# Kernel tuning notes

Measured on AMD Instinct MI355X. Metric: run time of the kernel, lower is better.

## Reference

```python
import jax, jax.numpy as jnp
import numpy as np

B, S, TK, N = 16, 32, 128, 512  # batch, sentences, tokens/sentence, 2*hidden_dim


def setup_inputs() -> dict:
    key = jax.random.key(0)
    ks = jax.random.split(key, 10)
    h = jax.random.normal(ks[0], (B, S, TK, N), dtype=jnp.float32)
    s_t_hat = jax.random.normal(ks[1], (B, N), dtype=jnp.float32)
    coverage = jax.random.uniform(ks[2], (B, S, TK), dtype=jnp.float32)
    # binary padding mask (mostly ones)
    enc_padding_mask = (jax.random.uniform(ks[3], (B, S, TK)) > 0.1).astype(jnp.float32)
    beta = jax.random.uniform(ks[4], (B, S), dtype=jnp.float32)
    sc = 1.0 / np.sqrt(N).astype(np.float32)
    W_h = jax.random.normal(ks[5], (N, N), dtype=jnp.float32) * sc   # Linear(N,N,bias=False)
    W_c = jax.random.normal(ks[6], (N,), dtype=jnp.float32)          # Linear(1,N,bias=False) weight[:,0]
    W_d = jax.random.normal(ks[7], (N, N), dtype=jnp.float32) * sc   # decode_proj weight
    b_d = jax.random.normal(ks[8], (N,), dtype=jnp.float32) * sc     # decode_proj bias
    v = jax.random.normal(ks[9], (N,), dtype=jnp.float32) * sc       # v weight[0]
    return {"s_t_hat": s_t_hat, "h": h, "coverage": coverage,
            "enc_padding_mask": enc_padding_mask, "beta": beta,
            "W_h": W_h, "W_c": W_c, "W_d": W_d, "b_d": b_d, "v": v}


def reference(s_t_hat, h, coverage, enc_padding_mask, beta, W_h, W_c, W_d, b_d, v):
    b, s, t_k, n = h.shape
    # encoder features: (b,s,t_k,n) @ W_h^T
    encoder_feature = jnp.einsum('bstn,mn->bstm', h, W_h)
    # decoder projection, broadcast over (s, t_k)
    dec_fea = s_t_hat @ W_d.T + b_d                              # (b, n)
    att_features = encoder_feature + dec_fea[:, None, None, :]
    # coverage feature: Linear(1, n) applied to coverage scalar
    att_features = att_features + coverage[..., None] * W_c     # (b,s,t_k,n)
    # scalar scores via v()
    scores = jnp.einsum('bstn,n->bst', jnp.tanh(att_features), v)
    # beta-weighted scores, flatten sentence/token dims
    weighted = (beta[:, :, None] * scores).reshape(b, s * t_k)
    mask_flat = enc_padding_mask.reshape(b, s * t_k)
    attn_ = jax.nn.softmax(weighted, axis=1) * mask_flat
    attn_dist = attn_ / attn_.sum(axis=1, keepdims=True)         # (b, s*t_k)
    # context vector
    c_t = jnp.einsum('bl,bln->bn', attn_dist, h.reshape(b, s * t_k, n))
    coverage_new = coverage + attn_dist.reshape(b, s, t_k)
    return c_t, attn_dist, coverage_new
```

## Files before the change

### kernel.cpp

```cpp
#include <hip/hip_runtime.h>
#include <hip/hip_bf16.h>

#define BB   16
#define SS   32
#define TKK  128
#define NN   512
#define LPB  4096
#define RPB  64

using bf16x8 = __attribute__((ext_vector_type(8))) __bf16;
using f32x4  = __attribute__((ext_vector_type(4))) float;

__device__ inline unsigned pack_bf16(float a, float b) {
  unsigned ua = __float_as_uint(a);
  unsigned ub = __float_as_uint(b);
  ua = (ua + 0x7FFFu + ((ua >> 16) & 1u)) >> 16;
  ub = (ub + 0x7FFFu + ((ub >> 16) & 1u)) >> 16;
  return ua | (ub << 16);
}

__device__ inline float tanh_fast(float x) {
  float e = __expf(2.0f * x);
  return 1.0f - 2.0f * __builtin_amdgcn_rcpf(e + 1.0f);
}

__global__ void prep_kernel(const float* __restrict__ W_h, uint4* __restrict__ Wpack,
                            const float* __restrict__ s_t_hat,
                            const float* __restrict__ W_d,
                            const float* __restrict__ b_d,
                            float* __restrict__ decfea) {
  if (blockIdx.x < 128) {
    int idx  = blockIdx.x * 256 + threadIdx.x;
    int lane = idx & 63;
    int ks   = (idx >> 6) & 15;
    int mt   = idx >> 10;
    int m    = mt * 16 + (lane & 15);
    int k0   = ks * 32 + ((lane >> 4) << 2);
    const float* wr = W_h + m * NN;
    float a0 = wr[k0 + 0],  a1 = wr[k0 + 1],  a2 = wr[k0 + 2],  a3 = wr[k0 + 3];
    float b0 = wr[k0 + 16], b1 = wr[k0 + 17], b2 = wr[k0 + 18], b3 = wr[k0 + 19];
    uint4 o;
    o.x = pack_bf16(a0, a1); o.y = pack_bf16(a2, a3);
    o.z = pack_bf16(b0, b1); o.w = pack_bf16(b2, b3);
    Wpack[idx] = o;
  } else {
    int idx = (blockIdx.x - 128) * 256 + threadIdx.x;
    int b = idx >> 9, m = idx & 511;
    const float4* sp = reinterpret_cast<const float4*>(s_t_hat + b * NN);
    const float4* wp = reinterpret_cast<const float4*>(W_d + m * NN);
    float acc = 0.f;
    #pragma unroll 8
    for (int i = 0; i < NN / 4; ++i) {
      float4 a = sp[i], w = wp[i];
      acc += a.x * w.x + a.y * w.y + a.z * w.z + a.w * w.w;
    }
    decfea[idx] = acc + b_d[m];
  }
}

__global__ __launch_bounds__(512, 4)
void score_kernel(const float* __restrict__ h,
                  const float* __restrict__ coverage,
                  const float* __restrict__ beta,
                  const float* __restrict__ W_c,
                  const float* __restrict__ v,
                  const uint4* __restrict__ Wpack,
                  const float* __restrict__ decfea,
                  float* __restrict__ weighted) {
  __shared__ __align__(16) unsigned short Afrag[RPB * NN];
  int tid  = threadIdx.x;
  int rb   = blockIdx.x;
  int bidx = rb >> 6;
  const float* hblk = h + (size_t)rb * RPB * NN;

  uint2* Af2 = reinterpret_cast<uint2*>(Afrag);
  #pragma unroll
  for (int i = 0; i < 16; ++i) {
    int u     = i * 512 + tid;
    int g     = u & 1;
    int lane6 = (u >> 1) & 63;
    int ksrt  = u >> 7;
    int row   = ((ksrt >> 4) << 4) + (lane6 & 15);
    int k0    = (ksrt & 15) * 32 + g * 16 + ((lane6 >> 4) << 2);
    float4 hv = *reinterpret_cast<const float4*>(hblk + row * NN + k0);
    uint2 p;
    p.x = pack_bf16(hv.x, hv.y);
    p.y = pack_bf16(hv.z, hv.w);
    Af2[u] = p;
  }
  __syncthreads();

  int lane = tid & 63;
  int w    = tid >> 6;

  f32x4 acc[4][4];
  const f32x4 zz = {0.f, 0.f, 0.f, 0.f};
  #pragma unroll
  for (int q = 0; q < 4; ++q)
    #pragma unroll
    for (int rt = 0; rt < 4; ++rt) acc[q][rt] = zz;

  const bf16x8* Afv = reinterpret_cast<const bf16x8*>(Afrag);
  const bf16x8* Bv  = reinterpret_cast<const bf16x8*>(Wpack) + (size_t)(w * 4) * 16 * 64 + lane;

  bf16x8 bf[4];
  #pragma unroll
  for (int q = 0; q < 4; ++q)
    bf[q] = Bv[(q * 16 + 0) * 64];
  for (int ks = 0; ks < 16; ++ks) {
    bf16x8 af[4];
    #pragma unroll
    for (int rt = 0; rt < 4; ++rt)
      af[rt] = Afv[(rt * 16 + ks) * 64 + lane];
    bf16x8 bn[4];
    if (ks < 15) {
      #pragma unroll
      for (int q = 0; q < 4; ++q)
        bn[q] = Bv[(q * 16 + ks + 1) * 64];
    }
    #pragma unroll
    for (int q = 0; q < 4; ++q)
      #pragma unroll
      for (int rt = 0; rt < 4; ++rt)
        acc[q][rt] = __builtin_amdgcn_mfma_f32_16x16x32_bf16(af[rt], bf[q], acc[q][rt], 0, 0, 0);
    #pragma unroll
    for (int q = 0; q < 4; ++q) bf[q] = bn[q];
  }

  int col = lane & 15;
  int rhi = (lane >> 4) << 2;
  float cv[4][4];
  #pragma unroll
  for (int rt = 0; rt < 4; ++rt)
    #pragma unroll
    for (int r = 0; r < 4; ++r)
      cv[rt][r] = coverage[rb * RPB + rt * 16 + rhi + r];

  float sc[4][4] = {};
  #pragma unroll
  for (int q = 0; q < 4; ++q) {
    int m = (w * 4 + q) * 16 + col;
    float dv = decfea[bidx * NN + m];
    float wc = W_c[m];
    float vv = v[m];
    #pragma unroll
    for (int rt = 0; rt < 4; ++rt)
      #pragma unroll
      for (int r = 0; r < 4; ++r) {
        float x = acc[q][rt][r] + dv + cv[rt][r] * wc;
        sc[rt][r] += vv * tanh_fast(x);
      }
  }
  #pragma unroll
  for (int rt = 0; rt < 4; ++rt)
    #pragma unroll
    for (int r = 0; r < 4; ++r) {
      float s = sc[rt][r];
      s += __shfl_xor(s, 1);
      s += __shfl_xor(s, 2);
      s += __shfl_xor(s, 4);
      s += __shfl_xor(s, 8);
      sc[rt][r] = s;
    }

  __syncthreads();
  float* scorebuf = reinterpret_cast<float*>(Afrag);
  if (col == 0) {
    #pragma unroll
    for (int rt = 0; rt < 4; ++rt)
      #pragma unroll
      for (int r = 0; r < 4; ++r)
        scorebuf[w * RPB + rt * 16 + rhi + r] = sc[rt][r];
  }
  __syncthreads();
  if (tid < RPB) {
    float total = 0.f;
    #pragma unroll
    for (int ww = 0; ww < 8; ++ww) total += scorebuf[ww * RPB + tid];
    int gl = rb * RPB + tid;
    int lb = gl & (LPB - 1);
    int s  = lb >> 7;
    weighted[bidx * LPB + lb] = beta[bidx * SS + s] * total;
  }
}

__global__ void softmax_kernel(const float* __restrict__ coverage,
                               const float* __restrict__ mask,
                               float* __restrict__ out) {
  int b = blockIdx.x;
  int t = threadIdx.x;
  float* ct   = out;
  float* attn = out + 8192;
  float* covn = out + 8192 + 65536;

  ct[b * NN + t] = 0.f;
  ct[b * NN + 256 + t] = 0.f;

  float wv[16];
  float mx = -1e30f;
  #pragma unroll
  for (int i = 0; i < 16; ++i) {
    wv[i] = attn[b * LPB + i * 256 + t];
    mx = fmaxf(mx, wv[i]);
  }
  __shared__ float redm[4], reds[4];
  mx = fmaxf(mx, __shfl_xor(mx, 1));
  mx = fmaxf(mx, __shfl_xor(mx, 2));
  mx = fmaxf(mx, __shfl_xor(mx, 4));
  mx = fmaxf(mx, __shfl_xor(mx, 8));
  mx = fmaxf(mx, __shfl_xor(mx, 16));
  mx = fmaxf(mx, __shfl_xor(mx, 32));
  if ((t & 63) == 0) redm[t >> 6] = mx;
  __syncthreads();
  mx = fmaxf(fmaxf(redm[0], redm[1]), fmaxf(redm[2], redm[3]));

  float e[16];
  float sum = 0.f;
  #pragma unroll
  for (int i = 0; i < 16; ++i) {
    e[i] = __expf(wv[i] - mx) * mask[b * LPB + i * 256 + t];
    sum += e[i];
  }
  sum += __shfl_xor(sum, 1);
  sum += __shfl_xor(sum, 2);
  sum += __shfl_xor(sum, 4);
  sum += __shfl_xor(sum, 8);
  sum += __shfl_xor(sum, 16);
  sum += __shfl_xor(sum, 32);
  if ((t & 63) == 0) reds[t >> 6] = sum;
  __syncthreads();
  sum = reds[0] + reds[1] + reds[2] + reds[3];
  float inv = 1.0f / sum;
  #pragma unroll
  for (int i = 0; i < 16; ++i) {
    int l = i * 256 + t;
    float a = e[i] * inv;
    attn[b * LPB + l] = a;
    covn[b * LPB + l] = coverage[b * LPB + l] + a;
  }
}

__global__ void ct_kernel(const float* __restrict__ h, float* __restrict__ out) {
  int blk   = blockIdx.x;
  int b     = blk >> 6;
  int chunk = blk & 63;
  int t     = threadIdx.x;
  const float* attn = out + 8192 + b * LPB + chunk * 64;
  __shared__ float as_[64];
  if (t < 64) as_[t] = attn[t];
  __syncthreads();
  const float* hp = h + (size_t)(b * LPB + chunk * 64) * NN;
  float a0 = 0.f, a1 = 0.f;
  #pragma unroll 4
  for (int r = 0; r < 64; ++r) {
    float2 hv = *reinterpret_cast<const float2*>(hp + r * NN + t * 2);
    float av = as_[r];
    a0 += av * hv.x;
    a1 += av * hv.y;
  }
  atomicAdd(&out[b * NN + t * 2],     a0);
  atomicAdd(&out[b * NN + t * 2 + 1], a1);
}

extern "C" void kernel_launch(void* const* d_in, const int* in_sizes, int n_in,
                              void* d_out, int out_size, void* d_ws, size_t ws_size,
                              hipStream_t stream) {
  const float* s_t_hat  = (const float*)d_in[0];
  const float* h        = (const float*)d_in[1];
  const float* coverage = (const float*)d_in[2];
  const float* mask     = (const float*)d_in[3];
  const float* beta     = (const float*)d_in[4];
  const float* W_h      = (const float*)d_in[5];
  const float* W_c      = (const float*)d_in[6];
  const float* W_d      = (const float*)d_in[7];
  const float* b_d      = (const float*)d_in[8];
  const float* v        = (const float*)d_in[9];
  float* out = (float*)d_out;

  uint4* Wpack    = (uint4*)d_ws;
  float* decfea   = out + 8192 + 65536;
  float* weighted = out + 8192;

  prep_kernel <<<160, 256, 0, stream>>>(W_h, Wpack, s_t_hat, W_d, b_d, decfea);
  score_kernel<<<1024, 512, 0, stream>>>(h, coverage, beta, W_c, v, Wpack, decfea, weighted);
  softmax_kernel<<<16, 256, 0, stream>>>(coverage, mask, out);
  ct_kernel<<<1024, 256, 0, stream>>>(h, out);
}
```

Baseline: 105.1 us.

## Coalesce h/W_h loads into XOR-swizzled LDS fragments and widen ct_kernel loads

The h tile is now staged into shared memory with full-row float4 loads, two per thread, and written to MFMA fragment order through an XOR swizzle. The old staging read scattered 16-byte pieces. The fragment reads use the same swizzle, which is meant to avoid LDS bank conflicts. The W_h packing moves to 8 larger blocks that use the same LDS transpose, and ct_kernel reads float4 over two row-interleaved halves. The cost is extra index arithmetic, fewer prep blocks, and twice as many atomics per thread in ct_kernel.

```diff
diff --git a/kernel.cpp b/kernel.cpp
--- a/kernel.cpp
+++ b/kernel.cpp
@@ -24,27 +24,42 @@
   return 1.0f - 2.0f * __builtin_amdgcn_rcpf(e + 1.0f);
 }
 
-__global__ void prep_kernel(const float* __restrict__ W_h, uint4* __restrict__ Wpack,
-                            const float* __restrict__ s_t_hat,
-                            const float* __restrict__ W_d,
-                            const float* __restrict__ b_d,
-                            float* __restrict__ decfea) {
-  if (blockIdx.x < 128) {
-    int idx  = blockIdx.x * 256 + threadIdx.x;
-    int lane = idx & 63;
-    int ks   = (idx >> 6) & 15;
-    int mt   = idx >> 10;
-    int m    = mt * 16 + (lane & 15);
-    int k0   = ks * 32 + ((lane >> 4) << 2);
-    const float* wr = W_h + m * NN;
-    float a0 = wr[k0 + 0],  a1 = wr[k0 + 1],  a2 = wr[k0 + 2],  a3 = wr[k0 + 3];
-    float b0 = wr[k0 + 16], b1 = wr[k0 + 17], b2 = wr[k0 + 18], b3 = wr[k0 + 19];
-    uint4 o;
-    o.x = pack_bf16(a0, a1); o.y = pack_bf16(a2, a3);
-    o.z = pack_bf16(b0, b1); o.w = pack_bf16(b2, b3);
-    Wpack[idx] = o;
+__device__ inline int swz(int f) { return f ^ ((f >> 4) & 15); }
+
+__global__ __launch_bounds__(512)
+void prep_kernel(const float* __restrict__ W_h, uint4* __restrict__ Wpack,
+                 const float* __restrict__ s_t_hat,
+                 const float* __restrict__ W_d,
+                 const float* __restrict__ b_d,
+                 float* __restrict__ decfea) {
+  __shared__ __align__(16) uint4 Wf[4096];
+  int tid = threadIdx.x;
+  if (blockIdx.x < 8) {
+    int tile = blockIdx.x;
+    const float4* wblk = reinterpret_cast<const float4*>(W_h + (size_t)tile * 64 * NN);
+    #pragma unroll
+    for (int i = 0; i < 8; ++i) {
+      int u   = i * 512 + tid;
+      int row = u >> 6;
+      int ks  = (u >> 2) & 15;
+      int lh  = u & 3;
+      int fb  = row * 128 + ks * 8 + lh;
+      float4 h0 = wblk[fb];
+      float4 h1 = wblk[fb + 4];
+      int frag = ((row >> 4) * 16 + ks) * 64 + lh * 16 + (row & 15);
+      uint4 o;
+      o.x = pack_bf16(h0.x, h0.y); o.y = pack_bf16(h0.z, h0.w);
+      o.z = pack_bf16(h1.x, h1.y); o.w = pack_bf16(h1.z, h1.w);
+      Wf[swz(frag)] = o;
+    }
+    __syncthreads();
+    #pragma unroll
+    for (int i = 0; i < 8; ++i) {
+      int f = i * 512 + tid;
+      Wpack[tile * 4096 + f] = Wf[swz(f)];
+    }
   } else {
-    int idx = (blockIdx.x - 128) * 256 + threadIdx.x;
+    int idx = (blockIdx.x - 8) * 512 + tid;
     int b = idx >> 9, m = idx & 511;
     const float4* sp = reinterpret_cast<const float4*>(s_t_hat + b * NN);
     const float4* wp = reinterpret_cast<const float4*>(W_d + m * NN);
@@ -71,22 +86,23 @@
   int tid  = threadIdx.x;
   int rb   = blockIdx.x;
   int bidx = rb >> 6;
-  const float* hblk = h + (size_t)rb * RPB * NN;
-
-  uint2* Af2 = reinterpret_cast<uint2*>(Afrag);
-  #pragma unroll
-  for (int i = 0; i < 16; ++i) {
-    int u     = i * 512 + tid;
-    int g     = u & 1;
-    int lane6 = (u >> 1) & 63;
-    int ksrt  = u >> 7;
-    int row   = ((ksrt >> 4) << 4) + (lane6 & 15);
-    int k0    = (ksrt & 15) * 32 + g * 16 + ((lane6 >> 4) << 2);
-    float4 hv = *reinterpret_cast<const float4*>(hblk + row * NN + k0);
-    uint2 p;
-    p.x = pack_bf16(hv.x, hv.y);
-    p.y = pack_bf16(hv.z, hv.w);
-    Af2[u] = p;
+  const float4* hblk4 = reinterpret_cast<const float4*>(h + (size_t)rb * RPB * NN);
+
+  uint4* Af4 = reinterpret_cast<uint4*>(Afrag);
+  #pragma unroll
+  for (int i = 0; i < 8; ++i) {
+    int u   = i * 512 + tid;
+    int row = u >> 6;
+    int ks  = (u >> 2) & 15;
+    int lh  = u & 3;
+    int fb  = row * 128 + ks * 8 + lh;
+    float4 h0 = hblk4[fb];
+    float4 h1 = hblk4[fb + 4];
+    int frag = ((row >> 4) * 16 + ks) * 64 + lh * 16 + (row & 15);
+    uint4 o;
+    o.x = pack_bf16(h0.x, h0.y); o.y = pack_bf16(h0.z, h0.w);
+    o.z = pack_bf16(h1.x, h1.y); o.w = pack_bf16(h1.z, h1.w);
+    Af4[swz(frag)] = o;
   }
   __syncthreads();
 
@@ -107,11 +123,14 @@
   #pragma unroll
   for (int q = 0; q < 4; ++q)
     bf[q] = Bv[(q * 16 + 0) * 64];
+  #pragma unroll 4
   for (int ks = 0; ks < 16; ++ks) {
     bf16x8 af[4];
     #pragma unroll
-    for (int rt = 0; rt < 4; ++rt)
-      af[rt] = Afv[(rt * 16 + ks) * 64 + lane];
+    for (int rt = 0; rt < 4; ++rt) {
+      int f = (rt * 16 + ks) * 64 + lane;
+      af[rt] = Afv[swz(f)];
+    }
     bf16x8 bn[4];
     if (ks < 15) {
       #pragma unroll
@@ -249,17 +268,20 @@
   __shared__ float as_[64];
   if (t < 64) as_[t] = attn[t];
   __syncthreads();
-  const float* hp = h + (size_t)(b * LPB + chunk * 64) * NN;
-  float a0 = 0.f, a1 = 0.f;
-  #pragma unroll 4
-  for (int r = 0; r < 64; ++r) {
-    float2 hv = *reinterpret_cast<const float2*>(hp + r * NN + t * 2);
+  int cg = t & 127;
+  int r0 = t >> 7;
+  const float4* hp = reinterpret_cast<const float4*>(h + (size_t)(b * LPB + chunk * 64) * NN);
+  float ax = 0.f, ay = 0.f, az = 0.f, aw = 0.f;
+  #pragma unroll 8
+  for (int r = r0; r < 64; r += 2) {
+    float4 hv = hp[r * 128 + cg];
     float av = as_[r];
-    a0 += av * hv.x;
-    a1 += av * hv.y;
-  }
-  atomicAdd(&out[b * NN + t * 2],     a0);
-  atomicAdd(&out[b * NN + t * 2 + 1], a1);
+    ax += av * hv.x; ay += av * hv.y; az += av * hv.z; aw += av * hv.w;
+  }
+  atomicAdd(&out[b * NN + cg * 4 + 0], ax);
+  atomicAdd(&out[b * NN + cg * 4 + 1], ay);
+  atomicAdd(&out[b * NN + cg * 4 + 2], az);
+  atomicAdd(&out[b * NN + cg * 4 + 3], aw);
 }
 
 extern "C" void kernel_launch(void* const* d_in, const int* in_sizes, int n_in,
@@ -281,7 +303,7 @@
   float* decfea   = out + 8192 + 65536;
   float* weighted = out + 8192;
 
-  prep_kernel <<<160, 256, 0, stream>>>(W_h, Wpack, s_t_hat, W_d, b_d, decfea);
+  prep_kernel <<<24, 512, 0, stream>>>(W_h, Wpack, s_t_hat, W_d, b_d, decfea);
   score_kernel<<<1024, 512, 0, stream>>>(h, coverage, beta, W_c, v, Wpack, decfea, weighted);
   softmax_kernel<<<16, 256, 0, stream>>>(coverage, mask, out);
   ct_kernel<<<1024, 256, 0, stream>>>(h, out);
```

New measurement: 138.8 us. 1.32x slower.
